# Performance work log

Measured on AMD Instinct MI355X. Metric: run time of the kernel, lower is better.

The kernel has to match this reference:

```python
import jax, jax.numpy as jnp
import numpy as np

N_POINTS = 50000
IN_DIM = 16
HID = 64
HEADS = 4
SCALE = 1
NEG_SLOPE = 0.2  # PyG GATConv default
DELTAS = [1, 3, 5, 7, 9, 11]


def _make_graphs(n, scale):
    # edge_index_1: edges (i-d, i); edge_index_2: edges (i+d, i); edge_index_3: both
    e1 = np.concatenate([np.stack([np.arange(d * scale, n) - d * scale,
                                   np.arange(d * scale, n)]) for d in DELTAS], axis=1)
    e2 = np.concatenate([np.stack([np.arange(n - d * scale) + d * scale,
                                   np.arange(n - d * scale)]) for d in DELTAS], axis=1)
    e3 = np.concatenate([e1, e2], axis=1)
    return (jnp.asarray(e1, dtype=jnp.int64), jnp.asarray(e2, dtype=jnp.int64),
            jnp.asarray(e3, dtype=jnp.int64))


def setup_inputs() -> dict:
    key = jax.random.key(0)
    ks = jax.random.split(key, 16)
    e1, e2, e3 = _make_graphs(N_POINTS, SCALE)
    HC = HEADS * HID

    def g(k, shape, fan_in):
        return jax.random.normal(k, shape, dtype=jnp.float32) * (1.0 / np.sqrt(fan_in))

    return {
        "x": jax.random.normal(ks[0], (N_POINTS, IN_DIM), dtype=jnp.float32),
        "edge_index_1": e1,
        "edge_index_2": e2,
        "edge_index_3": e3,
        # stacked params for the 3 branches (leading dim 3)
        "W1": g(ks[1], (3, IN_DIM, HC), IN_DIM),
        "a1_src": g(ks[2], (3, HEADS, HID), HID),
        "a1_dst": g(ks[3], (3, HEADS, HID), HID),
        "b1": jnp.zeros((3, HC), dtype=jnp.float32),
        "W2": g(ks[4], (3, HC, HC), HC),
        "a2_src": g(ks[5], (3, HEADS, HID), HID),
        "a2_dst": g(ks[6], (3, HEADS, HID), HID),
        "b2": jnp.zeros((3, HID), dtype=jnp.float32),
        "W_fc": g(ks[7], (3, HID, 1), HID),
        "b_fc": jnp.zeros((3, 1), dtype=jnp.float32),
    }


def _gat(x, src, dst, W, a_src, a_dst, b, concat):
    """PyG GATConv: linear -> edge attention -> scatter-softmax -> scatter-add."""
    N = x.shape[0]
    H, C = a_src.shape
    h = (x @ W).reshape(N, H, C)                      # [N,H,C]
    # add self loops (PyG default add_self_loops=True; input graphs have none)
    loop = jnp.arange(N, dtype=src.dtype)
    src = jnp.concatenate([src, loop])
    dst = jnp.concatenate([dst, loop])
    alpha_s = (h * a_src).sum(-1)                     # [N,H]
    alpha_d = (h * a_dst).sum(-1)                     # [N,H]
    e = jax.nn.leaky_relu(alpha_s[src] + alpha_d[dst], NEG_SLOPE)  # [E,H]
    m = jax.ops.segment_max(e, dst, num_segments=N)   # per-dst max (stable softmax)
    ex = jnp.exp(e - m[dst])
    den = jax.ops.segment_sum(ex, dst, num_segments=N)
    alpha = ex / den[dst]                             # [E,H]
    out = jax.ops.segment_sum(alpha[:, :, None] * h[src], dst, num_segments=N)  # [N,H,C]
    out = out.reshape(N, H * C) if concat else out.mean(axis=1)
    return out + b


def reference(x, edge_index_1, edge_index_2, edge_index_3,
              W1, a1_src, a1_dst, b1, W2, a2_src, a2_dst, b2, W_fc, b_fc):
    eis = [edge_index_1, edge_index_2, edge_index_3]
    outs = []
    for k in range(3):
        src, dst = eis[k][0], eis[k][1]
        h = _gat(x, src, dst, W1[k], a1_src[k], a1_dst[k], b1[k], concat=True)
        h = _gat(h, src, dst, W2[k], a2_src[k], a2_dst[k], b2[k], concat=False)
        outs.append(h @ W_fc[k] + b_fc[k])            # [N,1]
    return tuple(outs)  # training-mode output (x1, x2, x3)
```

## Files before the change

kernel.cpp:

```cpp
#include <hip/hip_runtime.h>

#define NPTS 50000
#define NEG 0.2f
#define PSTRIDE 960
#define OUT_N 196
#define SPAN_A 240
#define SPAN_B 218
#define STRA 240
#define LOG2E 1.44269504088896340736f

typedef unsigned short u16;
typedef unsigned int   u32;

__device__ __forceinline__ float bf2f(u16 u){ return __uint_as_float(((u32)u) << 16); }
__device__ __forceinline__ u16 f2bf(float f){
  u32 w = __float_as_uint(f);
  return (u16)((w + 0x7fffu + ((w >> 16) & 1u)) >> 16);
}
__device__ __forceinline__ u32 pk2(float a, float b){
  return (u32)f2bf(a) | ((u32)f2bf(b) << 16);
}
__device__ __forceinline__ float ldraw(const void* p, long i, int isf32){
  return isf32 ? ((const float*)p)[i] : bf2f(((const u16*)p)[i]);
}
__device__ __forceinline__ float wred(float v){
  #pragma unroll
  for (int m = 32; m > 0; m >>= 1) v += __shfl_xor(v, m, 64);
  return v;
}

__device__ int detect_isf32(const void* x){
  int lane = threadIdx.x & 63;
  const u16* p = (const u16*)x;
  int ze = 0, sane = 0;
  #pragma unroll
  for (int r = 0; r < 8; r++){
    int idx = lane * 8 + r;
    u16 u = p[idx];
    if ((idx & 1) == 0 && u == 0) ze++;
    float a = fabsf(bf2f(u));
    if (u == 0 || (a > 0.015625f && a < 64.f)) sane++;
  }
  #pragma unroll
  for (int m = 32; m > 0; m >>= 1){ ze += __shfl_xor(ze, m, 64); sane += __shfl_xor(sane, m, 64); }
  return (ze > 200) ? 1 : (sane > 460 ? 0 : 1);
}

template<int B> __device__ __forceinline__ int nbr_off(int t){
  if (B == 0){ constexpr int O[7]  = {0,-1,-3,-5,-7,-9,-11}; return O[t]; }
  else if (B == 1){ constexpr int O[7]  = {0,1,3,5,7,9,11}; return O[t]; }
  else { constexpr int O[13] = {0,-1,1,-3,3,-5,5,-7,7,-9,9,-11,11}; return O[t]; }
}

__global__ __launch_bounds__(256) void k_fold1(const void* x, const void* W2, const void* a2s,
                                               const void* a2d, const void* wfc, float* sAg){
  __shared__ int s_flag;
  if (threadIdx.x < 64){ int f = detect_isf32(x); if (threadIdx.x == 0) s_flag = f; }
  __syncthreads();
  int isf32 = s_flag;
  int kb = blockIdx.y, m = blockIdx.x;
  int hp = threadIdx.x >> 6, ch = threadIdx.x & 63;
  int c = hp * 64 + ch;
  float w = ldraw(W2, (long)kb * 65536 + (long)m * 256 + c, isf32);
  float s = wred(w * ldraw(a2s, kb * 256 + c, isf32));
  float d = wred(w * ldraw(a2d, kb * 256 + c, isf32));
  float f = wred(w * ldraw(wfc, kb * 64 + ch, isf32) * 0.25f);
  if (ch == 0){
    float* sA = sAg + (long)kb * 3072;
    sA[(0 * 4 + hp) * 256 + m] = s;
    sA[(1 * 4 + hp) * 256 + m] = d;
    sA[(2 * 4 + hp) * 256 + m] = f;
  }
}

__global__ __launch_bounds__(256) void k_fold2(const void* x, const void* W1, const void* a1s,
                                               const void* a1d, const void* b1, const void* b2,
                                               const void* wfc, const void* bfc,
                                               const float* sAg, float* P){
  __shared__ int s_flag;
  if (threadIdx.x < 64){ int f = detect_isf32(x); if (threadIdx.x == 0) s_flag = f; }
  __syncthreads();
  int isf32 = s_flag;
  int kb = blockIdx.y;
  int wid = blockIdx.x * 4 + (threadIdx.x >> 6);
  int ch = threadIdx.x & 63;
  float* Pp = P + kb * PSTRIDE;
  const float* sA = sAg + (long)kb * 3072;

  if (wid < 256){
    int hp = wid & 3, h = (wid >> 2) & 3, k = wid >> 4;
    int m = h * 64 + ch;
    float w = ldraw(W1, (long)kb * 4096 + k * 256 + m, isf32);
    float s = wred(w * sA[(0 * 4 + hp) * 256 + m]);
    float d = wred(w * sA[(1 * 4 + hp) * 256 + m]);
    float f = wred(w * sA[(2 * 4 + hp) * 256 + m]);
    if (ch == 0){ Pp[128 + wid] = s; Pp[384 + wid] = d; Pp[640 + wid] = f; }
  } else if (wid < 320){
    int j = wid - 256; int h = j & 3, k = j >> 2;
    int c = h * 64 + ch;
    float w = ldraw(W1, (long)kb * 4096 + k * 256 + c, isf32);
    float s = wred(w * ldraw(a1s, kb * 256 + c, isf32));
    float d = wred(w * ldraw(a1d, kb * 256 + c, isf32));
    if (ch == 0){ Pp[j] = s; Pp[64 + j] = d; }
  } else if (wid < 324){
    int hp = wid - 320;
    float a0 = 0.f, a1v = 0.f, a2v = 0.f;
    for (int it = 0; it < 4; it++){
      int m = it * 64 + ch;
      float bv = ldraw(b1, kb * 256 + m, isf32);
      a0  += bv * sA[(0 * 4 + hp) * 256 + m];
      a1v += bv * sA[(1 * 4 + hp) * 256 + m];
      a2v += bv * sA[(2 * 4 + hp) * 256 + m];
    }
    a0 = wred(a0); a1v = wred(a1v); a2v = wred(a2v);
    if (ch == 0){ Pp[896 + hp] = a0; Pp[900 + hp] = a1v; Pp[904 + hp] = a2v; }
  } else if (wid == 324){
    float a = wred(ldraw(b2, kb * 64 + ch, isf32) * ldraw(wfc, kb * 64 + ch, isf32));
    if (ch == 0) Pp[908] = a + ldraw(bfc, kb, isf32);
  }
}

template<int BRANCH>
__device__ __forceinline__ void run_main(const void* x, void* out, int isf32, int base,
                                         float (&sP)[912], float (&fe8)[8][STRA],
                                         u32 (&feG)[4][STRA][7], float (&o2)[12][STRA]){
  constexpr int CNT = (BRANCH == 2) ? 13 : 7;
  int tid = threadIdx.x;

  if (tid < SPAN_A){
    int g = base - 22 + tid;
    bool vA = (unsigned)g < NPTS;
    float xv[16];
    if (vA){
      if (isf32){
        const float4* xp = (const float4*)x + (long)g * 4;
        #pragma unroll
        for (int q = 0; q < 4; q++){
          float4 v = xp[q];
          xv[q*4] = v.x; xv[q*4+1] = v.y; xv[q*4+2] = v.z; xv[q*4+3] = v.w;
        }
      } else {
        const uint4* xp = (const uint4*)x + (long)g * 2;
        #pragma unroll
        for (int q = 0; q < 2; q++){
          uint4 v = xp[q];
          u32 wsv[4] = {v.x, v.y, v.z, v.w};
          #pragma unroll
          for (int r = 0; r < 4; r++){
            xv[q*8 + r*2]     = bf2f((u16)(wsv[r] & 0xffffu));
            xv[q*8 + r*2 + 1] = bf2f((u16)(wsv[r] >> 16));
          }
        }
      }
    } else {
      #pragma unroll
      for (int k = 0; k < 16; k++) xv[k] = 0.f;
    }
    float s1[4] = {0,0,0,0}, d1[4] = {0,0,0,0};
    float s2[16], d2[16], f2[16];
    #pragma unroll
    for (int t = 0; t < 16; t++){ s2[t] = 0.f; d2[t] = 0.f; f2[t] = 0.f; }
    #pragma unroll
    for (int k = 0; k < 16; k++){
      float xk = xv[k];
      float4 a = *(const float4*)&sP[k * 4];
      s1[0] += xk * a.x; s1[1] += xk * a.y; s1[2] += xk * a.z; s1[3] += xk * a.w;
      float4 b = *(const float4*)&sP[64 + k * 4];
      d1[0] += xk * b.x; d1[1] += xk * b.y; d1[2] += xk * b.z; d1[3] += xk * b.w;
      #pragma unroll
      for (int q = 0; q < 4; q++){
        float4 vs = *(const float4*)&sP[128 + k * 16 + q * 4];
        s2[q*4] += xk * vs.x; s2[q*4+1] += xk * vs.y; s2[q*4+2] += xk * vs.z; s2[q*4+3] += xk * vs.w;
        float4 vd = *(const float4*)&sP[384 + k * 16 + q * 4];
        d2[q*4] += xk * vd.x; d2[q*4+1] += xk * vd.y; d2[q*4+2] += xk * vd.z; d2[q*4+3] += xk * vd.w;
        float4 vf = *(const float4*)&sP[640 + k * 16 + q * 4];
        f2[q*4] += xk * vf.x; f2[q*4+1] += xk * vf.y; f2[q*4+2] += xk * vf.z; f2[q*4+3] += xk * vf.w;
      }
    }
    #pragma unroll
    for (int h = 0; h < 4; h++){
      fe8[h][tid] = s1[h] * LOG2E;
      fe8[4 + h][tid] = d1[h] * LOG2E;
      feG[h][tid][0] = pk2(s2[h*4+0], s2[h*4+1]);
      feG[h][tid][1] = pk2(s2[h*4+2], s2[h*4+3]);
      feG[h][tid][2] = pk2(d2[h*4+0], d2[h*4+1]);
      feG[h][tid][3] = pk2(d2[h*4+2], d2[h*4+3]);
      feG[h][tid][4] = pk2(f2[h*4+0], f2[h*4+1]);
      feG[h][tid][5] = pk2(f2[h*4+2], f2[h*4+3]);
    }
  }
  __syncthreads();

  #pragma unroll
  for (int pass = 0; pass < 4; pass++){
    int task = pass * 256 + tid;
    if (task < SPAN_B * 4){
      int slotB = task >> 2, h = task & 3;
      int gB = base - 11 + slotB;
      bool vB = (unsigned)gB < NPTS;
      float ts[4] = {0,0,0,0}, td[4] = {0,0,0,0}, tf[4] = {0,0,0,0};
      if (vB){
        int sAs = slotB + 11;
        float adv = fe8[4 + h][sAs];
        float e[CNT]; int sa[CNT];
        float mx = -3e38f;
        #pragma unroll
        for (int tt = 0; tt < CNT; tt++){
          int off = nbr_off<BRANCH>(tt);
          int j = gB + off;
          sa[tt] = sAs + off;
          float v = fe8[h][sa[tt]] + adv;
          v = v > 0.f ? v : NEG * v;
          e[tt] = ((unsigned)j < NPTS) ? v : -3e38f;
          mx = fmaxf(mx, e[tt]);
        }
        float den = 0.f;
        #pragma unroll
        for (int tt = 0; tt < CNT; tt++){
          float ex = exp2f(e[tt] - mx);
          den += ex;
          const u32* gp = &feG[h][sa[tt]][0];
          u32 g0 = gp[0], g1 = gp[1], g2 = gp[2], g3 = gp[3], g4 = gp[4], g5 = gp[5];
          ts[0] += ex * bf2f((u16)(g0 & 0xffffu)); ts[1] += ex * bf2f((u16)(g0 >> 16));
          ts[2] += ex * bf2f((u16)(g1 & 0xffffu)); ts[3] += ex * bf2f((u16)(g1 >> 16));
          td[0] += ex * bf2f((u16)(g2 & 0xffffu)); td[1] += ex * bf2f((u16)(g2 >> 16));
          td[2] += ex * bf2f((u16)(g3 & 0xffffu)); td[3] += ex * bf2f((u16)(g3 >> 16));
          tf[0] += ex * bf2f((u16)(g4 & 0xffffu)); tf[1] += ex * bf2f((u16)(g4 >> 16));
          tf[2] += ex * bf2f((u16)(g5 & 0xffffu)); tf[3] += ex * bf2f((u16)(g5 >> 16));
        }
        float inv = 1.f / den;
        #pragma unroll
        for (int hp = 0; hp < 4; hp++){ ts[hp] *= inv; td[hp] *= inv; tf[hp] *= inv; }
      }
      #pragma unroll
      for (int hp = 0; hp < 4; hp++){
        ts[hp] += __shfl_xor(ts[hp], 1, 64); ts[hp] += __shfl_xor(ts[hp], 2, 64);
        td[hp] += __shfl_xor(td[hp], 1, 64); td[hp] += __shfl_xor(td[hp], 2, 64);
        tf[hp] += __shfl_xor(tf[hp], 1, 64); tf[hp] += __shfl_xor(tf[hp], 2, 64);
      }
      if (h == 0){
        #pragma unroll
        for (int hp = 0; hp < 4; hp++){
          o2[hp][slotB]     = vB ? (ts[hp] + sP[896 + hp]) * LOG2E : 0.f;
          o2[4 + hp][slotB] = vB ? (td[hp] + sP[900 + hp]) * LOG2E : 0.f;
          o2[8 + hp][slotB] = vB ? tf[hp] + sP[904 + hp] : 0.f;
        }
      }
    }
  }
  __syncthreads();

  #pragma unroll
  for (int pass = 0; pass < 4; pass++){
    int task = pass * 256 + tid;
    if (task < OUT_N * 4){
      int offn = task >> 2, hp = task & 3;
      int i = base + offn;
      bool vC = i < NPTS;
      float r = 0.f;
      if (vC){
        int sBs = offn + 11;
        float adv = o2[4 + hp][sBs];
        float e[CNT]; int sb[CNT];
        float mx = -3e38f;
        #pragma unroll
        for (int tt = 0; tt < CNT; tt++){
          int off = nbr_off<BRANCH>(tt);
          int j = i + off;
          sb[tt] = sBs + off;
          float v = o2[hp][sb[tt]] + adv;
          v = v > 0.f ? v : NEG * v;
          e[tt] = ((unsigned)j < NPTS) ? v : -3e38f;
          mx = fmaxf(mx, e[tt]);
        }
        float den = 0.f, sm = 0.f;
        #pragma unroll
        for (int tt = 0; tt < CNT; tt++){
          float ex = exp2f(e[tt] - mx);
          den += ex;
          sm += ex * o2[8 + hp][sb[tt]];
        }
        r = sm / den;
      }
      r += __shfl_xor(r, 1, 64);
      r += __shfl_xor(r, 2, 64);
      if (hp == 0 && vC){
        float o = r + sP[908];
        long oi = (long)BRANCH * NPTS + i;
        if (isf32) ((float*)out)[oi] = o;
        else       ((u16*)out)[oi]  = f2bf(o);
      }
    }
  }
}

__global__ __launch_bounds__(256) void k_main(const void* x, const float* P, void* out){
  __shared__ float sP[912];
  __shared__ float fe8[8][STRA];
  __shared__ u32 feG[4][STRA][7];
  __shared__ float o2[12][STRA];
  __shared__ int s_flag;
  int tid = threadIdx.x;
  int br = blockIdx.y;
  if (tid < 64){ int f = detect_isf32(x); if (tid == 0) s_flag = f; }
  for (int i = tid; i < 912; i += 256) sP[i] = P[br * PSTRIDE + i];
  __syncthreads();
  int isf32 = s_flag;
  int base = blockIdx.x * OUT_N;
  if (br == 0)      run_main<0>(x, out, isf32, base, sP, fe8, feG, o2);
  else if (br == 1) run_main<1>(x, out, isf32, base, sP, fe8, feG, o2);
  else              run_main<2>(x, out, isf32, base, sP, fe8, feG, o2);
}

extern "C" void kernel_launch(void* const* d_in, const int* in_sizes, int n_in,
                              void* d_out, int out_size, void* d_ws, size_t ws_size,
                              hipStream_t stream){
  char* ws = (char*)d_ws;
  size_t off = 0;
  auto take = [&](size_t b) -> size_t { size_t r = off; off += (b + 255) & ~(size_t)255; return r; };

  float* sAg = (float*)(ws + take((size_t)3 * 3072 * 4));
  float* P   = (float*)(ws + take((size_t)3 * PSTRIDE * 4));

  const void* x   = d_in[0];
  const void* W1  = d_in[4];
  const void* a1s = d_in[5];
  const void* a1d = d_in[6];
  const void* b1  = d_in[7];
  const void* W2  = d_in[8];
  const void* a2s = d_in[9];
  const void* a2d = d_in[10];
  const void* b2  = d_in[11];
  const void* wfc = d_in[12];
  const void* bfc = d_in[13];

  k_fold1<<<dim3(256, 3), 256, 0, stream>>>(x, W2, a2s, a2d, wfc, sAg);
  k_fold2<<<dim3(82, 3), 256, 0, stream>>>(x, W1, a1s, a1d, b1, b2, wfc, bfc, sAg, P);
  k_main<<<dim3((NPTS + OUT_N - 1) / OUT_N, 3), 256, 0, stream>>>(x, P, d_out);
}
```

Measured before the change: 64.14 us.

## Shrink main tiles, read params from global, hoist dtype flag into fold kernel

Output tile per block shrinks from 196 to 96 points, giving more blocks and smaller shared arrays with odd strides to reduce bank conflicts. The per-block dtype detection and shared-memory parameter staging are removed: fold1 writes the dtype flag once and the main kernel reads parameters straight from global/scalar memory. Out-of-range x loads are clamped instead of branched, and bf16 unpacking and packing use cheaper bit operations and intrinsics. In exchange, halo overhead per tile rises (22 extra rows on 96 outputs instead of 196).

Result: slower. 75.85 us (+18.3%).

```diff
diff --git a/kernel.cpp b/kernel.cpp
--- a/kernel.cpp
+++ b/kernel.cpp
@@ -1,12 +1,14 @@
 #include <hip/hip_runtime.h>
+#include <hip/hip_bf16.h>
 
 #define NPTS 50000
 #define NEG 0.2f
 #define PSTRIDE 960
-#define OUT_N 196
-#define SPAN_A 240
-#define SPAN_B 218
-#define STRA 240
+#define OUT_N 96
+#define SPAN_A 140
+#define SPAN_B 118
+#define SAP 141
+#define OSTR 119
 #define LOG2E 1.44269504088896340736f
 
 typedef unsigned short u16;
@@ -18,8 +20,12 @@
   return (u16)((w + 0x7fffu + ((w >> 16) & 1u)) >> 16);
 }
 __device__ __forceinline__ u32 pk2(float a, float b){
-  return (u32)f2bf(a) | ((u32)f2bf(b) << 16);
-}
+  __hip_bfloat162 h2 = __float22bfloat162_rn(float2{a, b});
+  union { __hip_bfloat162 h; u32 u; } cv; cv.h = h2;
+  return cv.u;
+}
+__device__ __forceinline__ float ulo(u32 g){ return __uint_as_float(g << 16); }
+__device__ __forceinline__ float uhi(u32 g){ return __uint_as_float(g & 0xffff0000u); }
 __device__ __forceinline__ float ldraw(const void* p, long i, int isf32){
   return isf32 ? ((const float*)p)[i] : bf2f(((const u16*)p)[i]);
 }
@@ -53,11 +59,13 @@
 }
 
 __global__ __launch_bounds__(256) void k_fold1(const void* x, const void* W2, const void* a2s,
-                                               const void* a2d, const void* wfc, float* sAg){
+                                               const void* a2d, const void* wfc, float* sAg,
+                                               int* flag){
   __shared__ int s_flag;
   if (threadIdx.x < 64){ int f = detect_isf32(x); if (threadIdx.x == 0) s_flag = f; }
   __syncthreads();
   int isf32 = s_flag;
+  if (blockIdx.x == 0 && blockIdx.y == 0 && threadIdx.x == 0) *flag = isf32;
   int kb = blockIdx.y, m = blockIdx.x;
   int hp = threadIdx.x >> 6, ch = threadIdx.x & 63;
   int c = hp * 64 + ch;
@@ -121,40 +129,35 @@
 }
 
 template<int BRANCH>
-__device__ __forceinline__ void run_main(const void* x, void* out, int isf32, int base,
-                                         float (&sP)[912], float (&fe8)[8][STRA],
-                                         u32 (&feG)[4][STRA][7], float (&o2)[12][STRA]){
+__device__ __forceinline__ void run_main(const void* x, const float* Pp, int isf32, int base,
+                                         float (&fe8)[8][SAP], u32 (&feG)[4][SAP * 7],
+                                         float (&o2)[12][OSTR], void* out){
   constexpr int CNT = (BRANCH == 2) ? 13 : 7;
   int tid = threadIdx.x;
 
   if (tid < SPAN_A){
     int g = base - 22 + tid;
-    bool vA = (unsigned)g < NPTS;
+    int gc = g < 0 ? 0 : (g >= NPTS ? NPTS - 1 : g);
     float xv[16];
-    if (vA){
-      if (isf32){
-        const float4* xp = (const float4*)x + (long)g * 4;
-        #pragma unroll
-        for (int q = 0; q < 4; q++){
-          float4 v = xp[q];
-          xv[q*4] = v.x; xv[q*4+1] = v.y; xv[q*4+2] = v.z; xv[q*4+3] = v.w;
-        }
-      } else {
-        const uint4* xp = (const uint4*)x + (long)g * 2;
-        #pragma unroll
-        for (int q = 0; q < 2; q++){
-          uint4 v = xp[q];
-          u32 wsv[4] = {v.x, v.y, v.z, v.w};
-          #pragma unroll
-          for (int r = 0; r < 4; r++){
-            xv[q*8 + r*2]     = bf2f((u16)(wsv[r] & 0xffffu));
-            xv[q*8 + r*2 + 1] = bf2f((u16)(wsv[r] >> 16));
-          }
-        }
+    if (isf32){
+      const float4* xp = (const float4*)x + (long)gc * 4;
+      #pragma unroll
+      for (int q = 0; q < 4; q++){
+        float4 v = xp[q];
+        xv[q*4] = v.x; xv[q*4+1] = v.y; xv[q*4+2] = v.z; xv[q*4+3] = v.w;
       }
     } else {
-      #pragma unroll
-      for (int k = 0; k < 16; k++) xv[k] = 0.f;
+      const uint4* xp = (const uint4*)x + (long)gc * 2;
+      #pragma unroll
+      for (int q = 0; q < 2; q++){
+        uint4 v = xp[q];
+        u32 wsv[4] = {v.x, v.y, v.z, v.w};
+        #pragma unroll
+        for (int r = 0; r < 4; r++){
+          xv[q*8 + r*2]     = ulo(wsv[r]);
+          xv[q*8 + r*2 + 1] = uhi(wsv[r]);
+        }
+      }
     }
     float s1[4] = {0,0,0,0}, d1[4] = {0,0,0,0};
     float s2[16], d2[16], f2[16];
@@ -163,36 +166,35 @@
     #pragma unroll
     for (int k = 0; k < 16; k++){
       float xk = xv[k];
-      float4 a = *(const float4*)&sP[k * 4];
-      s1[0] += xk * a.x; s1[1] += xk * a.y; s1[2] += xk * a.z; s1[3] += xk * a.w;
-      float4 b = *(const float4*)&sP[64 + k * 4];
-      d1[0] += xk * b.x; d1[1] += xk * b.y; d1[2] += xk * b.z; d1[3] += xk * b.w;
-      #pragma unroll
-      for (int q = 0; q < 4; q++){
-        float4 vs = *(const float4*)&sP[128 + k * 16 + q * 4];
-        s2[q*4] += xk * vs.x; s2[q*4+1] += xk * vs.y; s2[q*4+2] += xk * vs.z; s2[q*4+3] += xk * vs.w;
-        float4 vd = *(const float4*)&sP[384 + k * 16 + q * 4];
-        d2[q*4] += xk * vd.x; d2[q*4+1] += xk * vd.y; d2[q*4+2] += xk * vd.z; d2[q*4+3] += xk * vd.w;
-        float4 vf = *(const float4*)&sP[640 + k * 16 + q * 4];
-        f2[q*4] += xk * vf.x; f2[q*4+1] += xk * vf.y; f2[q*4+2] += xk * vf.z; f2[q*4+3] += xk * vf.w;
+      #pragma unroll
+      for (int h = 0; h < 4; h++){
+        s1[h] += xk * Pp[     k*4 + h];
+        d1[h] += xk * Pp[64 + k*4 + h];
+      }
+      #pragma unroll
+      for (int t = 0; t < 16; t++){
+        s2[t] += xk * Pp[128 + k*16 + t];
+        d2[t] += xk * Pp[384 + k*16 + t];
+        f2[t] += xk * Pp[640 + k*16 + t];
       }
     }
     #pragma unroll
     for (int h = 0; h < 4; h++){
-      fe8[h][tid] = s1[h] * LOG2E;
+      fe8[h][tid]     = s1[h] * LOG2E;
       fe8[4 + h][tid] = d1[h] * LOG2E;
-      feG[h][tid][0] = pk2(s2[h*4+0], s2[h*4+1]);
-      feG[h][tid][1] = pk2(s2[h*4+2], s2[h*4+3]);
-      feG[h][tid][2] = pk2(d2[h*4+0], d2[h*4+1]);
-      feG[h][tid][3] = pk2(d2[h*4+2], d2[h*4+3]);
-      feG[h][tid][4] = pk2(f2[h*4+0], f2[h*4+1]);
-      feG[h][tid][5] = pk2(f2[h*4+2], f2[h*4+3]);
+      u32* gp = &feG[h][tid * 7];
+      gp[0] = pk2(s2[h*4+0], s2[h*4+1]);
+      gp[1] = pk2(s2[h*4+2], s2[h*4+3]);
+      gp[2] = pk2(d2[h*4+0], d2[h*4+1]);
+      gp[3] = pk2(d2[h*4+2], d2[h*4+3]);
+      gp[4] = pk2(f2[h*4+0], f2[h*4+1]);
+      gp[5] = pk2(f2[h*4+2], f2[h*4+3]);
     }
   }
   __syncthreads();
 
   #pragma unroll
-  for (int pass = 0; pass < 4; pass++){
+  for (int pass = 0; pass < 2; pass++){
     int task = pass * 256 + tid;
     if (task < SPAN_B * 4){
       int slotB = task >> 2, h = task & 3;
@@ -219,14 +221,14 @@
         for (int tt = 0; tt < CNT; tt++){
           float ex = exp2f(e[tt] - mx);
           den += ex;
-          const u32* gp = &feG[h][sa[tt]][0];
+          const u32* gp = &feG[h][sa[tt] * 7];
           u32 g0 = gp[0], g1 = gp[1], g2 = gp[2], g3 = gp[3], g4 = gp[4], g5 = gp[5];
-          ts[0] += ex * bf2f((u16)(g0 & 0xffffu)); ts[1] += ex * bf2f((u16)(g0 >> 16));
-          ts[2] += ex * bf2f((u16)(g1 & 0xffffu)); ts[3] += ex * bf2f((u16)(g1 >> 16));
-          td[0] += ex * bf2f((u16)(g2 & 0xffffu)); td[1] += ex * bf2f((u16)(g2 >> 16));
-          td[2] += ex * bf2f((u16)(g3 & 0xffffu)); td[3] += ex * bf2f((u16)(g3 >> 16));
-          tf[0] += ex * bf2f((u16)(g4 & 0xffffu)); tf[1] += ex * bf2f((u16)(g4 >> 16));
-          tf[2] += ex * bf2f((u16)(g5 & 0xffffu)); tf[3] += ex * bf2f((u16)(g5 >> 16));
+          ts[0] += ex * ulo(g0); ts[1] += ex * uhi(g0);
+          ts[2] += ex * ulo(g1); ts[3] += ex * uhi(g1);
+          td[0] += ex * ulo(g2); td[1] += ex * uhi(g2);
+          td[2] += ex * ulo(g3); td[3] += ex * uhi(g3);
+          tf[0] += ex * ulo(g4); tf[1] += ex * uhi(g4);
+          tf[2] += ex * ulo(g5); tf[3] += ex * uhi(g5);
         }
         float inv = 1.f / den;
         #pragma unroll
@@ -241,9 +243,9 @@
       if (h == 0){
         #pragma unroll
         for (int hp = 0; hp < 4; hp++){
-          o2[hp][slotB]     = vB ? (ts[hp] + sP[896 + hp]) * LOG2E : 0.f;
-          o2[4 + hp][slotB] = vB ? (td[hp] + sP[900 + hp]) * LOG2E : 0.f;
-          o2[8 + hp][slotB] = vB ? tf[hp] + sP[904 + hp] : 0.f;
+          o2[hp][slotB]     = vB ? (ts[hp] + Pp[896 + hp]) * LOG2E : 0.f;
+          o2[4 + hp][slotB] = vB ? (td[hp] + Pp[900 + hp]) * LOG2E : 0.f;
+          o2[8 + hp][slotB] = vB ? tf[hp] + Pp[904 + hp] : 0.f;
         }
       }
     }
@@ -251,7 +253,7 @@
   __syncthreads();
 
   #pragma unroll
-  for (int pass = 0; pass < 4; pass++){
+  for (int pass = 0; pass < 2; pass++){
     int task = pass * 256 + tid;
     if (task < OUT_N * 4){
       int offn = task >> 2, hp = task & 3;
@@ -285,7 +287,7 @@
       r += __shfl_xor(r, 1, 64);
       r += __shfl_xor(r, 2, 64);
       if (hp == 0 && vC){
-        float o = r + sP[908];
+        float o = r + Pp[908];
         long oi = (long)BRANCH * NPTS + i;
         if (isf32) ((float*)out)[oi] = o;
         else       ((u16*)out)[oi]  = f2bf(o);
@@ -294,22 +296,18 @@
   }
 }
 
-__global__ __launch_bounds__(256) void k_main(const void* x, const float* P, void* out){
-  __shared__ float sP[912];
-  __shared__ float fe8[8][STRA];
-  __shared__ u32 feG[4][STRA][7];
-  __shared__ float o2[12][STRA];
-  __shared__ int s_flag;
-  int tid = threadIdx.x;
+__global__ __launch_bounds__(256) void k_main(const void* x, const float* P, const int* flag,
+                                              void* out){
+  __shared__ float fe8[8][SAP];
+  __shared__ u32 feG[4][SAP * 7];
+  __shared__ float o2[12][OSTR];
   int br = blockIdx.y;
-  if (tid < 64){ int f = detect_isf32(x); if (tid == 0) s_flag = f; }
-  for (int i = tid; i < 912; i += 256) sP[i] = P[br * PSTRIDE + i];
-  __syncthreads();
-  int isf32 = s_flag;
+  int isf32 = *flag;
+  const float* Pp = P + br * PSTRIDE;
   int base = blockIdx.x * OUT_N;
-  if (br == 0)      run_main<0>(x, out, isf32, base, sP, fe8, feG, o2);
-  else if (br == 1) run_main<1>(x, out, isf32, base, sP, fe8, feG, o2);
-  else              run_main<2>(x, out, isf32, base, sP, fe8, feG, o2);
+  if (br == 0)      run_main<0>(x, Pp, isf32, base, fe8, feG, o2, out);
+  else if (br == 1) run_main<1>(x, Pp, isf32, base, fe8, feG, o2, out);
+  else              run_main<2>(x, Pp, isf32, base, fe8, feG, o2, out);
 }
 
 extern "C" void kernel_launch(void* const* d_in, const int* in_sizes, int n_in,
@@ -319,8 +317,9 @@
   size_t off = 0;
   auto take = [&](size_t b) -> size_t { size_t r = off; off += (b + 255) & ~(size_t)255; return r; };
 
-  float* sAg = (float*)(ws + take((size_t)3 * 3072 * 4));
-  float* P   = (float*)(ws + take((size_t)3 * PSTRIDE * 4));
+  float* sAg  = (float*)(ws + take((size_t)3 * 3072 * 4));
+  float* P    = (float*)(ws + take((size_t)3 * PSTRIDE * 4));
+  int*   flag = (int*)(ws + take(4));
 
   const void* x   = d_in[0];
   const void* W1  = d_in[4];
@@ -334,7 +333,7 @@
   const void* wfc = d_in[12];
   const void* bfc = d_in[13];
 
-  k_fold1<<<dim3(256, 3), 256, 0, stream>>>(x, W2, a2s, a2d, wfc, sAg);
+  k_fold1<<<dim3(256, 3), 256, 0, stream>>>(x, W2, a2s, a2d, wfc, sAg, flag);
   k_fold2<<<dim3(82, 3), 256, 0, stream>>>(x, W1, a1s, a1d, b1, b2, wfc, bfc, sAg, P);
-  k_main<<<dim3((NPTS + OUT_N - 1) / OUT_N, 3), 256, 0, stream>>>(x, P, d_out);
-}
+  k_main<<<dim3((NPTS + OUT_N - 1) / OUT_N, 3), 256, 0, stream>>>(x, P, flag, d_out);
+}
```
